# Kernel optimization log

Measured on AMD Instinct MI355X. Metric: run time of the kernel, lower is better.

## Reference

```python
import jax, jax.numpy as jnp
import numpy as np

EMBED_DIM = 1024
NUM_HEADS = 16
HEAD_DIM = EMBED_DIM // NUM_HEADS
WINDOW = 256
B, S = 2, 2048


def setup_inputs() -> dict:
    key = jax.random.key(0)
    ks = jax.random.split(key, 9)
    sc = 1.0 / np.sqrt(EMBED_DIM)
    inp = {
        "x": jax.random.normal(ks[0], (B, S, EMBED_DIM), dtype=jnp.float32),
        "Wq": jax.random.normal(ks[1], (EMBED_DIM, EMBED_DIM), dtype=jnp.float32) * sc,
        "Wk": jax.random.normal(ks[2], (EMBED_DIM, EMBED_DIM), dtype=jnp.float32) * sc,
        "Wv": jax.random.normal(ks[3], (EMBED_DIM, EMBED_DIM), dtype=jnp.float32) * sc,
        "Wo": jax.random.normal(ks[4], (EMBED_DIM, EMBED_DIM), dtype=jnp.float32) * sc,
        "bq": jax.random.normal(ks[5], (EMBED_DIM,), dtype=jnp.float32) * 0.01,
        "bk": jax.random.normal(ks[6], (EMBED_DIM,), dtype=jnp.float32) * 0.01,
        "bv": jax.random.normal(ks[7], (EMBED_DIM,), dtype=jnp.float32) * 0.01,
        "bo": jax.random.normal(ks[8], (EMBED_DIM,), dtype=jnp.float32) * 0.01,
    }
    return inp


def _sliding_window_mask(seq_len: int) -> jnp.ndarray:
    # True where attention is NOT permitted (future or beyond window)
    idx = jnp.arange(seq_len)
    rel = idx[None, :] - idx[:, None]  # (S, S): key_pos - query_pos
    return (rel > 0) | (rel < -WINDOW)


def reference(x, Wq, Wk, Wv, Wo, bq, bk, bv, bo):
    Bx, Sx, E = x.shape
    H, D = NUM_HEADS, HEAD_DIM
    # projections (torch Linear: y = x @ W.T + b)
    q = (x @ Wq.T + bq).reshape(Bx, Sx, H, D).transpose(0, 2, 1, 3)  # (B,H,S,D)
    k = (x @ Wk.T + bk).reshape(Bx, Sx, H, D).transpose(0, 2, 1, 3)
    v = (x @ Wv.T + bv).reshape(Bx, Sx, H, D).transpose(0, 2, 1, 3)
    q = q * (D ** -0.5)
    attn = jnp.einsum("bhqd,bhkd->bhqk", q, k)  # (B,H,S,S) dense scores
    mask = _sliding_window_mask(Sx)
    attn = jnp.where(mask, -jnp.inf, attn)
    attn = jax.nn.softmax(attn, axis=-1)
    y = jnp.einsum("bhqk,bhkd->bhqd", attn, v)
    y = y.transpose(0, 2, 1, 3).reshape(Bx, Sx, E)
    return y @ Wo.T + bo
```

## Files before the change

kernel.cpp:

```cpp
#include <hip/hip_runtime.h>

#define E_DIM 1024
#define NHEAD 16
#define HDIM 64
#define SEQ 2048
#define NBATCH 2
#define WIN 256
#define MTOK (NBATCH * SEQ)
#define BKT 32
#define NT (E_DIM / BKT)

typedef __attribute__((ext_vector_type(4))) float f32x4;
typedef __attribute__((ext_vector_type(8))) short short8;
typedef __attribute__((ext_vector_type(4))) unsigned short u16x4;

#define AS1 __attribute__((address_space(1)))
#define AS3 __attribute__((address_space(3)))

__device__ __forceinline__ void gll16(const void* g, void* l) {
    __builtin_amdgcn_global_load_lds((const AS1 void*)g, (AS3 void*)l, 16, 0, 0);
}

__device__ __forceinline__ unsigned short f2bf(float f) {
    union { float f; unsigned u; } a; a.f = f;
    unsigned r = a.u + 0x7fffu + ((a.u >> 16) & 1u);
    return (unsigned short)(r >> 16);
}

__global__ __launch_bounds__(256) void conv_f2b(const float* __restrict__ src,
                                                unsigned short* __restrict__ dst, int n4) {
    int i = blockIdx.x * 256 + threadIdx.x;
    int stride = gridDim.x * 256;
    for (; i < n4; i += stride) {
        float4 v = ((const float4*)src)[i];
        u16x4 o;
        o[0] = f2bf(v.x); o[1] = f2bf(v.y); o[2] = f2bf(v.z); o[3] = f2bf(v.w);
        ((u16x4*)dst)[i] = o;
    }
}

__global__ __launch_bounds__(256) void conv_w4(const float* __restrict__ w0, const float* __restrict__ w1,
                                               const float* __restrict__ w2, const float* __restrict__ w3,
                                               unsigned short* __restrict__ o0, unsigned short* __restrict__ o1,
                                               unsigned short* __restrict__ o2, unsigned short* __restrict__ o3) {
    const int m = blockIdx.y;
    const float* src = (m == 0) ? w0 : (m == 1) ? w1 : (m == 2) ? w2 : w3;
    unsigned short* dst = (m == 0) ? o0 : (m == 1) ? o1 : (m == 2) ? o2 : o3;
    int i = blockIdx.x * 256 + threadIdx.x;
    float4 v = ((const float4*)src)[i];
    u16x4 o;
    o[0] = f2bf(v.x); o[1] = f2bf(v.y); o[2] = f2bf(v.z); o[3] = f2bf(v.w);
    ((u16x4*)dst)[i] = o;
}

__global__ __launch_bounds__(512, 2) void gemm8_qkv(const unsigned short* __restrict__ xb,
        const unsigned short* __restrict__ wqb, const unsigned short* __restrict__ wkb,
        const unsigned short* __restrict__ wvb,
        const float* __restrict__ bq, const float* __restrict__ bk, const float* __restrict__ bv,
        unsigned short* __restrict__ qo, unsigned short* __restrict__ ko,
        unsigned short* __restrict__ vTo) {
    __shared__ char lds[131072];
    const int tid = threadIdx.x;
    const int w = tid >> 6, l = tid & 63;
    const int r16 = l & 15, kq = l >> 4;
    const int wm = w >> 2, wn = w & 3;
    const int m0 = blockIdx.x * 256;
    const int by = blockIdx.y;
    const int mat = by >> 2;
    const int nb = (by & 3) * 256;
    const unsigned short* Bw = (mat == 0) ? wqb : (mat == 1) ? wkb : wvb;

    const int srow = tid >> 2;
    const int sslot = tid & 3;
    const unsigned short* aSrc0 = xb + (size_t)(m0 + srow) * E_DIM + sslot * 8;
    const unsigned short* aSrc1 = aSrc0 + (size_t)128 * E_DIM;
    const unsigned short* bSrc0 = Bw + (size_t)(nb + srow) * E_DIM + sslot * 8;
    const unsigned short* bSrc1 = bSrc0 + (size_t)128 * E_DIM;
    const int dstOff = w * 1024;

#define STAGE_A(t) { char* d_ = lds + ((t) & 3) * 32768 + dstOff; \
                     gll16(aSrc0 + (t) * BKT, d_); gll16(aSrc1 + (t) * BKT, d_ + 8192); }
#define STAGE_B(t) { char* d_ = lds + ((t) & 3) * 32768 + 16384 + dstOff; \
                     gll16(bSrc0 + (t) * BKT, d_); gll16(bSrc1 + (t) * BKT, d_ + 8192); }

    f32x4 acc[8][4];
    #pragma unroll
    for (int m = 0; m < 8; ++m)
        #pragma unroll
        for (int n = 0; n < 4; ++n)
            acc[m][n] = (f32x4){0.f, 0.f, 0.f, 0.f};

    STAGE_A(0); STAGE_B(0); STAGE_A(1); STAGE_B(1);

    for (int t = 0; t < NT; ++t) {
        if (t < NT - 1) { asm volatile("s_waitcnt vmcnt(4)" ::: "memory"); }
        else            { asm volatile("s_waitcnt vmcnt(0)" ::: "memory"); }
        __builtin_amdgcn_sched_barrier(0);
        __builtin_amdgcn_s_barrier();
        __builtin_amdgcn_sched_barrier(0);
        char* la = lds + (t & 3) * 32768;
        char* lb = la + 16384;
        short8 bfr[4], af[4];
        #pragma unroll
        for (int n = 0; n < 4; ++n)
            bfr[n] = *(const short8*)(lb + (wn * 64 + n * 16 + r16) * 64 + kq * 16);
        #pragma unroll
        for (int j = 0; j < 4; ++j)
            af[j] = *(const short8*)(la + (wm * 128 + j * 16 + r16) * 64 + kq * 16);
        if (t + 2 < NT) STAGE_A(t + 2);
        __builtin_amdgcn_s_barrier();
        __builtin_amdgcn_sched_barrier(0);
        __builtin_amdgcn_s_setprio(1);
        #pragma unroll
        for (int j = 0; j < 4; ++j)
            #pragma unroll
            for (int n = 0; n < 4; ++n)
                acc[j][n] = __builtin_amdgcn_mfma_f32_16x16x32_bf16(af[j], bfr[n], acc[j][n], 0, 0, 0);
        __builtin_amdgcn_s_setprio(0);
        short8 af2[4];
        #pragma unroll
        for (int j = 0; j < 4; ++j)
            af2[j] = *(const short8*)(la + (wm * 128 + (4 + j) * 16 + r16) * 64 + kq * 16);
        if (t + 2 < NT) STAGE_B(t + 2);
        __builtin_amdgcn_s_barrier();
        __builtin_amdgcn_sched_barrier(0);
        __builtin_amdgcn_s_setprio(1);
        #pragma unroll
        for (int j = 0; j < 4; ++j)
            #pragma unroll
            for (int n = 0; n < 4; ++n)
                acc[4 + j][n] = __builtin_amdgcn_mfma_f32_16x16x32_bf16(af2[j], bfr[n], acc[4 + j][n], 0, 0, 0);
        __builtin_amdgcn_s_setprio(0);
    }
#undef STAGE_A
#undef STAGE_B

    const float* bias = (mat == 0) ? bq : (mat == 1) ? bk : bv;
    const float scale = (mat == 0) ? 0.125f : 1.0f;
    #pragma unroll
    for (int n = 0; n < 4; ++n) {
        int e = nb + wn * 64 + n * 16 + r16;
        float bb = bias[e];
        int h = e >> 6, d = e & 63;
        #pragma unroll
        for (int m = 0; m < 8; ++m) {
            int tok = m0 + wm * 128 + m * 16 + kq * 4;
            int b = tok >> 11, s = tok & (SEQ - 1);
            if (mat == 2) {
                u16x4 o;
                #pragma unroll
                for (int r = 0; r < 4; ++r) o[r] = f2bf(acc[m][n][r] + bb);
                *(u16x4*)(vTo + ((size_t)(b * NHEAD + h) * HDIM + d) * SEQ + s) = o;
            } else {
                unsigned short* dst = (mat == 0) ? qo : ko;
                #pragma unroll
                for (int r = 0; r < 4; ++r) {
                    float val = (acc[m][n][r] + bb) * scale;
                    dst[((size_t)(b * NHEAD + h) * SEQ + s + r) * HDIM + d] = f2bf(val);
                }
            }
        }
    }
}

__device__ __forceinline__ void gemm_tile(const unsigned short* __restrict__ A,
                                          const unsigned short* __restrict__ Bw,
                                          int m0, int n0,
                                          f32x4 acc[4][4], char* ldsA, char* ldsB) {
    const int t = threadIdx.x;
    const int w = t >> 6, l = t & 63;
    const int r16 = l & 15, kq = l >> 4;
    const int wr = w >> 1, wc = w & 1;
    const int srow = l >> 3, ps = l & 7;

    for (int kt = 0; kt < E_DIM / 64; ++kt) {
        #pragma unroll
        for (int c = 0; c < 4; ++c) {
            int chunk = w * 4 + c;
            int row = chunk * 8 + srow;
            int kslot = ps ^ (row & 7);
            gll16(A  + (size_t)(m0 + row) * E_DIM + kt * 64 + kslot * 8, ldsA + chunk * 1024);
            gll16(Bw + (size_t)(n0 + row) * E_DIM + kt * 64 + kslot * 8, ldsB + chunk * 1024);
        }
        __syncthreads();
        #pragma unroll
        for (int kk = 0; kk < 2; ++kk) {
            short8 af[4], bfr[4];
            #pragma unroll
            for (int m = 0; m < 4; ++m) {
                int rr = wr * 64 + m * 16 + r16;
                int c = kk * 4 + kq;
                af[m] = *(const short8*)(ldsA + rr * 128 + ((c ^ (rr & 7)) * 16));
            }
            #pragma unroll
            for (int n = 0; n < 4; ++n) {
                int rr = wc * 64 + n * 16 + r16;
                int c = kk * 4 + kq;
                bfr[n] = *(const short8*)(ldsB + rr * 128 + ((c ^ (rr & 7)) * 16));
            }
            #pragma unroll
            for (int m = 0; m < 4; ++m)
                #pragma unroll
                for (int n = 0; n < 4; ++n)
                    acc[m][n] = __builtin_amdgcn_mfma_f32_16x16x32_bf16(af[m], bfr[n], acc[m][n], 0, 0, 0);
        }
        __syncthreads();
    }
}

__global__ __launch_bounds__(256) void attn_swa(const unsigned short* __restrict__ q,
                                                const unsigned short* __restrict__ k,
                                                const unsigned short* __restrict__ vT,
                                                unsigned short* __restrict__ y) {
    __shared__ char plds[4 * 2048];
    const int t = threadIdx.x;
    const int w = t >> 6, l = t & 63;
    const int r16 = l & 15, kq = l >> 4;
    const int wid = blockIdx.x * 4 + w;
    const int bh = wid >> 7;
    const int q0 = (wid & 127) * 16;
    const unsigned short* qp = q + (size_t)bh * SEQ * HDIM;
    const unsigned short* kp = k + (size_t)bh * SEQ * HDIM;
    const unsigned short* vp = vT + (size_t)bh * HDIM * SEQ;
    char* pl = plds + w * 2048;

    short8 qf0 = *(const short8*)(qp + (q0 + r16) * HDIM + kq * 8);
    short8 qf1 = *(const short8*)(qp + (q0 + r16) * HDIM + 32 + kq * 8);

    f32x4 po[4];
    #pragma unroll
    for (int nn = 0; nn < 4; ++nn) po[nn] = (f32x4){0.f, 0.f, 0.f, 0.f};
    float mrow[4] = {-1e30f, -1e30f, -1e30f, -1e30f};
    float lrow[4] = {0.f, 0.f, 0.f, 0.f};

    const int kstart = (q0 >= WIN) ? ((q0 - WIN) & ~31) : 0;
    for (int k0 = kstart; k0 <= q0 + 15; k0 += 32) {
        f32x4 sc[2];
        #pragma unroll
        for (int n = 0; n < 2; ++n) {
            const unsigned short* kr = kp + (size_t)(k0 + n * 16 + r16) * HDIM + kq * 8;
            short8 kf0 = *(const short8*)(kr);
            short8 kf1 = *(const short8*)(kr + 32);
            f32x4 z = {0.f, 0.f, 0.f, 0.f};
            z = __builtin_amdgcn_mfma_f32_16x16x32_bf16(qf0, kf0, z, 0, 0, 0);
            sc[n] = __builtin_amdgcn_mfma_f32_16x16x32_bf16(qf1, kf1, z, 0, 0, 0);
        }
        float tmax[4];
        #pragma unroll
        for (int r = 0; r < 4; ++r) {
            int qrow = q0 + kq * 4 + r;
            int key0 = k0 + r16;
            int key1 = key0 + 16;
            if (!(key0 <= qrow && key0 >= qrow - WIN)) sc[0][r] = -1e30f;
            if (!(key1 <= qrow && key1 >= qrow - WIN)) sc[1][r] = -1e30f;
            tmax[r] = fmaxf(sc[0][r], sc[1][r]);
        }
        #pragma unroll
        for (int off = 1; off < 16; off <<= 1) {
            #pragma unroll
            for (int r = 0; r < 4; ++r)
                tmax[r] = fmaxf(tmax[r], __shfl_xor(tmax[r], off));
        }
        float pv0[4], pv1[4], psum[4];
        #pragma unroll
        for (int r = 0; r < 4; ++r) {
            float mnew = fmaxf(mrow[r], tmax[r]);
            float resc = __expf(mrow[r] - mnew);
            mrow[r] = mnew;
            lrow[r] *= resc;
            po[0][r] *= resc; po[1][r] *= resc; po[2][r] *= resc; po[3][r] *= resc;
            float p0 = (sc[0][r] > -1e29f) ? __expf(sc[0][r] - mnew) : 0.f;
            float p1 = (sc[1][r] > -1e29f) ? __expf(sc[1][r] - mnew) : 0.f;
            pv0[r] = p0; pv1[r] = p1;
            psum[r] = p0 + p1;
        }
        #pragma unroll
        for (int off = 1; off < 16; off <<= 1) {
            #pragma unroll
            for (int r = 0; r < 4; ++r)
                psum[r] += __shfl_xor(psum[r], off);
        }
        #pragma unroll
        for (int r = 0; r < 4; ++r) lrow[r] += psum[r];

        #pragma unroll
        for (int r = 0; r < 4; ++r) {
            int row = kq * 4 + r;
            int c0 = r16 ^ ((row & 7) << 3);
            int c1 = (16 + r16) ^ ((row & 7) << 3);
            *(unsigned short*)(pl + row * 128 + c0 * 2) = f2bf(pv0[r]);
            *(unsigned short*)(pl + row * 128 + c1 * 2) = f2bf(pv1[r]);
        }
        short8 pa = *(const short8*)(pl + r16 * 128 + ((kq ^ (r16 & 7)) * 16));
        #pragma unroll
        for (int nn = 0; nn < 4; ++nn) {
            short8 vf = *(const short8*)(vp + (size_t)(nn * 16 + r16) * SEQ + k0 + kq * 8);
            po[nn] = __builtin_amdgcn_mfma_f32_16x16x32_bf16(pa, vf, po[nn], 0, 0, 0);
        }
    }

    const int b = bh >> 4, h = bh & 15;
    #pragma unroll
    for (int nn = 0; nn < 4; ++nn) {
        #pragma unroll
        for (int r = 0; r < 4; ++r) {
            int s = q0 + kq * 4 + r;
            float val = po[nn][r] / lrow[r];
            y[((size_t)(b * SEQ + s)) * E_DIM + h * HDIM + nn * 16 + r16] = f2bf(val);
        }
    }
}

__global__ __launch_bounds__(256) void gemm_out(const unsigned short* __restrict__ yb,
        const unsigned short* __restrict__ wob, const float* __restrict__ bo,
        float* __restrict__ out) {
    __shared__ char lds[32768];
    const int m0 = blockIdx.x * 128;
    const int n0 = blockIdx.y * 128;
    f32x4 acc[4][4];
    #pragma unroll
    for (int m = 0; m < 4; ++m)
        #pragma unroll
        for (int n = 0; n < 4; ++n)
            acc[m][n] = (f32x4){0.f, 0.f, 0.f, 0.f};

    gemm_tile(yb, wob, m0, n0, acc, lds, lds + 16384);

    const int t = threadIdx.x;
    const int w = t >> 6, l = t & 63;
    const int r16 = l & 15, kq = l >> 4;
    const int wr = w >> 1, wc = w & 1;
    #pragma unroll
    for (int n = 0; n < 4; ++n) {
        int e = n0 + wc * 64 + n * 16 + r16;
        float bb = bo[e];
        #pragma unroll
        for (int m = 0; m < 4; ++m) {
            #pragma unroll
            for (int r = 0; r < 4; ++r) {
                int tok = m0 + wr * 64 + m * 16 + kq * 4 + r;
                out[(size_t)tok * E_DIM + e] = acc[m][n][r] + bb;
            }
        }
    }
}

extern "C" void kernel_launch(void* const* d_in, const int* in_sizes, int n_in,
                              void* d_out, int out_size, void* d_ws, size_t ws_size,
                              hipStream_t stream) {
    const float* x  = (const float*)d_in[0];
    const float* Wq = (const float*)d_in[1];
    const float* Wk = (const float*)d_in[2];
    const float* Wv = (const float*)d_in[3];
    const float* Wo = (const float*)d_in[4];
    const float* bq = (const float*)d_in[5];
    const float* bk = (const float*)d_in[6];
    const float* bv = (const float*)d_in[7];
    const float* bo = (const float*)d_in[8];
    float* out = (float*)d_out;

    char* ws = (char*)d_ws;
    unsigned short* xb  = (unsigned short*)(ws);
    unsigned short* wqb = (unsigned short*)(ws + ((size_t)8 << 20));
    unsigned short* wkb = (unsigned short*)(ws + ((size_t)10 << 20));
    unsigned short* wvb = (unsigned short*)(ws + ((size_t)12 << 20));
    unsigned short* wob = (unsigned short*)(ws + ((size_t)14 << 20));
    unsigned short* qw  = (unsigned short*)(ws + ((size_t)16 << 20));
    unsigned short* kw  = (unsigned short*)(ws + ((size_t)24 << 20));
    unsigned short* vTw = (unsigned short*)(ws + ((size_t)40 << 20));
    unsigned short* yw  = (unsigned short*)(ws + ((size_t)48 << 20));

    conv_f2b<<<4096, 256, 0, stream>>>(x, xb, MTOK * E_DIM / 4);
    conv_w4<<<dim3(1024, 4), 256, 0, stream>>>(Wq, Wk, Wv, Wo, wqb, wkb, wvb, wob);

    gemm8_qkv<<<dim3(16, 12), 512, 0, stream>>>(xb, wqb, wkb, wvb, bq, bk, bv, qw, kw, vTw);
    attn_swa<<<1024, 256, 0, stream>>>(qw, kw, vTw, yw);
    gemm_out<<<dim3(32, 8), 256, 0, stream>>>(yw, wob, bo, out);
}
```

Measured before the change: 188.0 us.

## Swizzle QKV GEMM LDS layout and process 32 query rows per attention wave

In the QKV GEMM, the global-to-LDS copy now permutes 16-byte chunk slots by an XOR of row bits, and the LDS fragment reads apply the same XOR, to cut LDS bank conflicts. The attention kernel now gives each wave two 16-row query fragments instead of one. Each K and V fragment loaded from global memory is reused for both, which halves the grid and the K/V traffic per query. The trade-off is higher register pressure and LDS use, plus fewer waves for latency hiding.

```diff
diff --git a/kernel.cpp b/kernel.cpp
--- a/kernel.cpp
+++ b/kernel.cpp
@@ -72,9 +72,11 @@
 
     const int srow = tid >> 2;
     const int sslot = tid & 3;
-    const unsigned short* aSrc0 = xb + (size_t)(m0 + srow) * E_DIM + sslot * 8;
+    const int fsw = (srow >> 1) & 3;
+    const int gslot = (sslot ^ fsw) * 8;
+    const unsigned short* aSrc0 = xb + (size_t)(m0 + srow) * E_DIM + gslot;
     const unsigned short* aSrc1 = aSrc0 + (size_t)128 * E_DIM;
-    const unsigned short* bSrc0 = Bw + (size_t)(nb + srow) * E_DIM + sslot * 8;
+    const unsigned short* bSrc0 = Bw + (size_t)(nb + srow) * E_DIM + gslot;
     const unsigned short* bSrc1 = bSrc0 + (size_t)128 * E_DIM;
     const int dstOff = w * 1024;
 
@@ -91,6 +93,9 @@
             acc[m][n] = (f32x4){0.f, 0.f, 0.f, 0.f};
 
     STAGE_A(0); STAGE_B(0); STAGE_A(1); STAGE_B(1);
+
+    const int fs = (r16 >> 1) & 3;
+    const int rdoff = (kq ^ fs) * 16;
 
     for (int t = 0; t < NT; ++t) {
         if (t < NT - 1) { asm volatile("s_waitcnt vmcnt(4)" ::: "memory"); }
@@ -103,10 +108,10 @@
         short8 bfr[4], af[4];
         #pragma unroll
         for (int n = 0; n < 4; ++n)
-            bfr[n] = *(const short8*)(lb + (wn * 64 + n * 16 + r16) * 64 + kq * 16);
+            bfr[n] = *(const short8*)(lb + (wn * 64 + n * 16 + r16) * 64 + rdoff);
         #pragma unroll
         for (int j = 0; j < 4; ++j)
-            af[j] = *(const short8*)(la + (wm * 128 + j * 16 + r16) * 64 + kq * 16);
+            af[j] = *(const short8*)(la + (wm * 128 + j * 16 + r16) * 64 + rdoff);
         if (t + 2 < NT) STAGE_A(t + 2);
         __builtin_amdgcn_s_barrier();
         __builtin_amdgcn_sched_barrier(0);
@@ -120,7 +125,7 @@
         short8 af2[4];
         #pragma unroll
         for (int j = 0; j < 4; ++j)
-            af2[j] = *(const short8*)(la + (wm * 128 + (4 + j) * 16 + r16) * 64 + kq * 16);
+            af2[j] = *(const short8*)(la + (wm * 128 + (4 + j) * 16 + r16) * 64 + rdoff);
         if (t + 2 < NT) STAGE_B(t + 2);
         __builtin_amdgcn_s_barrier();
         __builtin_amdgcn_sched_barrier(0);
@@ -212,103 +217,134 @@
                                                 const unsigned short* __restrict__ k,
                                                 const unsigned short* __restrict__ vT,
                                                 unsigned short* __restrict__ y) {
-    __shared__ char plds[4 * 2048];
+    __shared__ char plds[4 * 4096];
     const int t = threadIdx.x;
     const int w = t >> 6, l = t & 63;
     const int r16 = l & 15, kq = l >> 4;
     const int wid = blockIdx.x * 4 + w;
-    const int bh = wid >> 7;
-    const int q0 = (wid & 127) * 16;
+    const int bh = wid >> 6;
+    const int q0 = (wid & 63) * 32;
     const unsigned short* qp = q + (size_t)bh * SEQ * HDIM;
     const unsigned short* kp = k + (size_t)bh * SEQ * HDIM;
     const unsigned short* vp = vT + (size_t)bh * HDIM * SEQ;
-    char* pl = plds + w * 2048;
-
-    short8 qf0 = *(const short8*)(qp + (q0 + r16) * HDIM + kq * 8);
-    short8 qf1 = *(const short8*)(qp + (q0 + r16) * HDIM + 32 + kq * 8);
-
-    f32x4 po[4];
-    #pragma unroll
-    for (int nn = 0; nn < 4; ++nn) po[nn] = (f32x4){0.f, 0.f, 0.f, 0.f};
-    float mrow[4] = {-1e30f, -1e30f, -1e30f, -1e30f};
-    float lrow[4] = {0.f, 0.f, 0.f, 0.f};
-
-    const int kstart = (q0 >= WIN) ? ((q0 - WIN) & ~31) : 0;
-    for (int k0 = kstart; k0 <= q0 + 15; k0 += 32) {
-        f32x4 sc[2];
+    char* pl = plds + w * 4096;
+
+    short8 qf[2][2];
+    #pragma unroll
+    for (int mf = 0; mf < 2; ++mf) {
+        const unsigned short* qr = qp + (q0 + mf * 16 + r16) * HDIM + kq * 8;
+        qf[mf][0] = *(const short8*)(qr);
+        qf[mf][1] = *(const short8*)(qr + 32);
+    }
+
+    f32x4 po[2][4];
+    float mrow[2][4], lrow[2][4];
+    #pragma unroll
+    for (int mf = 0; mf < 2; ++mf) {
+        #pragma unroll
+        for (int nn = 0; nn < 4; ++nn) po[mf][nn] = (f32x4){0.f, 0.f, 0.f, 0.f};
+        #pragma unroll
+        for (int r = 0; r < 4; ++r) { mrow[mf][r] = -1e30f; lrow[mf][r] = 0.f; }
+    }
+
+    const int kstart = (q0 >= WIN) ? (q0 - WIN) : 0;
+    for (int k0 = kstart; k0 <= q0 + 31; k0 += 32) {
+        short8 kf[2][2];
         #pragma unroll
         for (int n = 0; n < 2; ++n) {
             const unsigned short* kr = kp + (size_t)(k0 + n * 16 + r16) * HDIM + kq * 8;
-            short8 kf0 = *(const short8*)(kr);
-            short8 kf1 = *(const short8*)(kr + 32);
-            f32x4 z = {0.f, 0.f, 0.f, 0.f};
-            z = __builtin_amdgcn_mfma_f32_16x16x32_bf16(qf0, kf0, z, 0, 0, 0);
-            sc[n] = __builtin_amdgcn_mfma_f32_16x16x32_bf16(qf1, kf1, z, 0, 0, 0);
-        }
-        float tmax[4];
-        #pragma unroll
-        for (int r = 0; r < 4; ++r) {
-            int qrow = q0 + kq * 4 + r;
-            int key0 = k0 + r16;
-            int key1 = key0 + 16;
-            if (!(key0 <= qrow && key0 >= qrow - WIN)) sc[0][r] = -1e30f;
-            if (!(key1 <= qrow && key1 >= qrow - WIN)) sc[1][r] = -1e30f;
-            tmax[r] = fmaxf(sc[0][r], sc[1][r]);
-        }
-        #pragma unroll
-        for (int off = 1; off < 16; off <<= 1) {
-            #pragma unroll
-            for (int r = 0; r < 4; ++r)
-                tmax[r] = fmaxf(tmax[r], __shfl_xor(tmax[r], off));
-        }
-        float pv0[4], pv1[4], psum[4];
-        #pragma unroll
-        for (int r = 0; r < 4; ++r) {
-            float mnew = fmaxf(mrow[r], tmax[r]);
-            float resc = __expf(mrow[r] - mnew);
-            mrow[r] = mnew;
-            lrow[r] *= resc;
-            po[0][r] *= resc; po[1][r] *= resc; po[2][r] *= resc; po[3][r] *= resc;
-            float p0 = (sc[0][r] > -1e29f) ? __expf(sc[0][r] - mnew) : 0.f;
-            float p1 = (sc[1][r] > -1e29f) ? __expf(sc[1][r] - mnew) : 0.f;
-            pv0[r] = p0; pv1[r] = p1;
-            psum[r] = p0 + p1;
-        }
-        #pragma unroll
-        for (int off = 1; off < 16; off <<= 1) {
-            #pragma unroll
-            for (int r = 0; r < 4; ++r)
-                psum[r] += __shfl_xor(psum[r], off);
-        }
-        #pragma unroll
-        for (int r = 0; r < 4; ++r) lrow[r] += psum[r];
-
-        #pragma unroll
-        for (int r = 0; r < 4; ++r) {
-            int row = kq * 4 + r;
-            int c0 = r16 ^ ((row & 7) << 3);
-            int c1 = (16 + r16) ^ ((row & 7) << 3);
-            *(unsigned short*)(pl + row * 128 + c0 * 2) = f2bf(pv0[r]);
-            *(unsigned short*)(pl + row * 128 + c1 * 2) = f2bf(pv1[r]);
-        }
-        short8 pa = *(const short8*)(pl + r16 * 128 + ((kq ^ (r16 & 7)) * 16));
+            kf[n][0] = *(const short8*)(kr);
+            kf[n][1] = *(const short8*)(kr + 32);
+        }
+        f32x4 sc[2][2];
+        #pragma unroll
+        for (int mf = 0; mf < 2; ++mf)
+            #pragma unroll
+            for (int n = 0; n < 2; ++n) {
+                f32x4 z = {0.f, 0.f, 0.f, 0.f};
+                z = __builtin_amdgcn_mfma_f32_16x16x32_bf16(qf[mf][0], kf[n][0], z, 0, 0, 0);
+                sc[mf][n] = __builtin_amdgcn_mfma_f32_16x16x32_bf16(qf[mf][1], kf[n][1], z, 0, 0, 0);
+            }
+        float tmax[2][4];
+        #pragma unroll
+        for (int mf = 0; mf < 2; ++mf)
+            #pragma unroll
+            for (int r = 0; r < 4; ++r) {
+                int qrow = q0 + mf * 16 + kq * 4 + r;
+                int key0 = k0 + r16;
+                int key1 = key0 + 16;
+                if (!(key0 <= qrow && key0 >= qrow - WIN)) sc[mf][0][r] = -1e30f;
+                if (!(key1 <= qrow && key1 >= qrow - WIN)) sc[mf][1][r] = -1e30f;
+                tmax[mf][r] = fmaxf(sc[mf][0][r], sc[mf][1][r]);
+            }
+        #pragma unroll
+        for (int off = 1; off < 16; off <<= 1)
+            #pragma unroll
+            for (int mf = 0; mf < 2; ++mf)
+                #pragma unroll
+                for (int r = 0; r < 4; ++r)
+                    tmax[mf][r] = fmaxf(tmax[mf][r], __shfl_xor(tmax[mf][r], off));
+        float pv[2][2][4], psum[2][4];
+        #pragma unroll
+        for (int mf = 0; mf < 2; ++mf)
+            #pragma unroll
+            for (int r = 0; r < 4; ++r) {
+                float mnew = fmaxf(mrow[mf][r], tmax[mf][r]);
+                float resc = __expf(mrow[mf][r] - mnew);
+                mrow[mf][r] = mnew;
+                lrow[mf][r] *= resc;
+                po[mf][0][r] *= resc; po[mf][1][r] *= resc;
+                po[mf][2][r] *= resc; po[mf][3][r] *= resc;
+                float p0 = (sc[mf][0][r] > -1e29f) ? __expf(sc[mf][0][r] - mnew) : 0.f;
+                float p1 = (sc[mf][1][r] > -1e29f) ? __expf(sc[mf][1][r] - mnew) : 0.f;
+                pv[mf][0][r] = p0; pv[mf][1][r] = p1;
+                psum[mf][r] = p0 + p1;
+            }
+        #pragma unroll
+        for (int off = 1; off < 16; off <<= 1)
+            #pragma unroll
+            for (int mf = 0; mf < 2; ++mf)
+                #pragma unroll
+                for (int r = 0; r < 4; ++r)
+                    psum[mf][r] += __shfl_xor(psum[mf][r], off);
+        #pragma unroll
+        for (int mf = 0; mf < 2; ++mf)
+            #pragma unroll
+            for (int r = 0; r < 4; ++r) lrow[mf][r] += psum[mf][r];
+
+        #pragma unroll
+        for (int mf = 0; mf < 2; ++mf)
+            #pragma unroll
+            for (int r = 0; r < 4; ++r) {
+                int row = kq * 4 + r;
+                int c0 = r16 ^ ((row & 7) << 3);
+                int c1 = (16 + r16) ^ ((row & 7) << 3);
+                *(unsigned short*)(pl + mf * 2048 + row * 128 + c0 * 2) = f2bf(pv[mf][0][r]);
+                *(unsigned short*)(pl + mf * 2048 + row * 128 + c1 * 2) = f2bf(pv[mf][1][r]);
+            }
+        short8 pa[2];
+        #pragma unroll
+        for (int mf = 0; mf < 2; ++mf)
+            pa[mf] = *(const short8*)(pl + mf * 2048 + r16 * 128 + ((kq ^ (r16 & 7)) * 16));
         #pragma unroll
         for (int nn = 0; nn < 4; ++nn) {
             short8 vf = *(const short8*)(vp + (size_t)(nn * 16 + r16) * SEQ + k0 + kq * 8);
-            po[nn] = __builtin_amdgcn_mfma_f32_16x16x32_bf16(pa, vf, po[nn], 0, 0, 0);
+            po[0][nn] = __builtin_amdgcn_mfma_f32_16x16x32_bf16(pa[0], vf, po[0][nn], 0, 0, 0);
+            po[1][nn] = __builtin_amdgcn_mfma_f32_16x16x32_bf16(pa[1], vf, po[1][nn], 0, 0, 0);
         }
     }
 
     const int b = bh >> 4, h = bh & 15;
     #pragma unroll
-    for (int nn = 0; nn < 4; ++nn) {
-        #pragma unroll
-        for (int r = 0; r < 4; ++r) {
-            int s = q0 + kq * 4 + r;
-            float val = po[nn][r] / lrow[r];
-            y[((size_t)(b * SEQ + s)) * E_DIM + h * HDIM + nn * 16 + r16] = f2bf(val);
-        }
-    }
+    for (int mf = 0; mf < 2; ++mf)
+        #pragma unroll
+        for (int nn = 0; nn < 4; ++nn)
+            #pragma unroll
+            for (int r = 0; r < 4; ++r) {
+                int s = q0 + mf * 16 + kq * 4 + r;
+                float val = po[mf][nn][r] / lrow[mf][r];
+                y[((size_t)(b * SEQ + s)) * E_DIM + h * HDIM + nn * 16 + r16] = f2bf(val);
+            }
 }
 
 __global__ __launch_bounds__(256) void gemm_out(const unsigned short* __restrict__ yb,
@@ -374,6 +410,6 @@
     conv_w4<<<dim3(1024, 4), 256, 0, stream>>>(Wq, Wk, Wv, Wo, wqb, wkb, wvb, wob);
 
     gemm8_qkv<<<dim3(16, 12), 512, 0, stream>>>(xb, wqb, wkb, wvb, bq, bk, bv, qw, kw, vTw);
-    attn_swa<<<1024, 256, 0, stream>>>(qw, kw, vTw, yw);
+    attn_swa<<<512, 256, 0, stream>>>(qw, kw, vTw, yw);
     gemm_out<<<dim3(32, 8), 256, 0, stream>>>(yw, wob, bo, out);
 }
```

Measured after the change: 177.3 us. -5.7%, faster.
